# Optimization experiments

Hardware: AMD Instinct MI355X
Metric: run time of the kernel (lower is better)

Reference implementation:

```python
import jax, jax.numpy as jnp
import numpy as np

ENERGY = 0.5  # target low-frequency energy ratio (init kwarg)
B, C, H, W = 8, 32, 512, 512


def setup_inputs() -> dict:
    key = jax.random.key(0)
    x = jax.random.normal(key, (B, C, H, W), dtype=jnp.float32)
    return {"x": x}


def reference(x) -> jnp.ndarray:
    b, c, h, w = x.shape
    crow, ccol = h // 2, w // 2

    f = jnp.fft.fft2(x)                       # [B,C,H,W] complex
    fshift = jnp.fft.fftshift(f, axes=(-2, -1))

    # Per-pixel minimal cutoff c such that pixel lies in the centered
    # square [crow-c:crow+c, ccol-c:ccol+c] (rows crow-c .. crow+c-1).
    ii = jnp.arange(h)
    jj = jnp.arange(w)
    c_row = jnp.maximum(crow - ii, ii - crow + 1)          # [H]
    c_col = jnp.maximum(ccol - jj, jj - ccol + 1)          # [W]
    c_needed = jnp.maximum(c_row[:, None], c_col[None, :])  # [H,W] int

    # Energy of channel 0 spectrum per batch element.
    e0 = jnp.abs(fshift[:, 0]) ** 2                         # [B,H,W]
    num_seg = int(max(crow, h - crow, ccol, w - ccol)) + 1
    seg = c_needed.reshape(-1)
    ring_energy = jax.vmap(
        lambda e: jax.ops.segment_sum(e.reshape(-1), seg, num_segments=num_seg)
    )(e0)                                                   # [B, num_seg]
    cum_energy = jnp.cumsum(ring_energy, axis=1)            # cum_energy[:, c] = low-freq energy at cutoff c
    total = cum_energy[:, -1]
    target = total * ENERGY

    # Search c in range(1, min(h,w)//2); first c with cum >= target, else 5.
    cmax = min(h, w) // 2
    cand = cum_energy[:, 1:cmax] >= target[:, None]          # [B, cmax-1]
    found = jnp.any(cand, axis=1)
    first = jnp.argmax(cand, axis=1) + 1                     # first satisfying cutoff
    cutoff = jnp.where(found, first, 5)                      # [B] int

    # Zero the centered square (same cutoff for all channels of a sample).
    keep = c_needed[None, :, :] > cutoff[:, None, None]      # [B,H,W] bool
    fshift = fshift * keep[:, None, :, :].astype(fshift.dtype)

    ishift = jnp.fft.ifftshift(fshift, axes=(-2, -1))
    return jnp.abs(jnp.fft.ifft2(ishift))
```

## Files before the change

kernel.cpp:

```cpp
#include <hip/hip_runtime.h>
#include <math.h>

#define FN 512
#define TPB 256
#define NIMG 256
#define NBATCH 8
#define NCH 32
#define NBINS 257
#define WACOLS 257
#define WBS 256
#define SPITCH 516

typedef unsigned long long ull;

__device__ __forceinline__ float2 cadd(float2 a, float2 b) { return make_float2(a.x + b.x, a.y + b.y); }
__device__ __forceinline__ float2 csub(float2 a, float2 b) { return make_float2(a.x - b.x, a.y - b.y); }
__device__ __forceinline__ float2 cmul(float2 a, float2 b) {
  return make_float2(fmaf(a.x, b.x, -a.y * b.y), fmaf(a.x, b.y, a.y * b.x));
}
template<bool INV>
__device__ __forceinline__ float2 cmul_s(float2 a, float2 w) {
  if (!INV) return make_float2(fmaf(a.x, w.x, -a.y * w.y), fmaf(a.x, w.y,  a.y * w.x));
  else      return make_float2(fmaf(a.x, w.x,  a.y * w.y), fmaf(a.y, w.x, -a.x * w.y));
}
__device__ __forceinline__ float2 cexpm(float ang) {
  float s, c;
  __sincosf(ang, &s, &c);
  return make_float2(c, s);
}
template<bool INV>
__device__ __forceinline__ float2 mulpmi(float2 a) {
  return INV ? make_float2(-a.y, a.x) : make_float2(a.y, -a.x);
}

template<bool INV>
__device__ __forceinline__ void dft8(float2 r[8]) {
  const float C = 0.70710678118654752440f;
  float2 t0 = cadd(r[0], r[4]), t1 = csub(r[0], r[4]);
  float2 t2 = cadd(r[2], r[6]), t3 = mulpmi<INV>(csub(r[2], r[6]));
  float2 E0 = cadd(t0, t2), E1 = cadd(t1, t3), E2 = csub(t0, t2), E3 = csub(t1, t3);
  float2 u0 = cadd(r[1], r[5]), u1 = csub(r[1], r[5]);
  float2 u2 = cadd(r[3], r[7]), u3 = mulpmi<INV>(csub(r[3], r[7]));
  float2 O0 = cadd(u0, u2), O1 = cadd(u1, u3), O2 = csub(u0, u2), O3 = csub(u1, u3);
  float2 O1w, O2w, O3w;
  if (!INV) {
    O1w = make_float2(C * (O1.x + O1.y), C * (O1.y - O1.x));
    O2w = make_float2(O2.y, -O2.x);
    O3w = make_float2(C * (O3.y - O3.x), -C * (O3.x + O3.y));
  } else {
    O1w = make_float2(C * (O1.x - O1.y), C * (O1.y + O1.x));
    O2w = make_float2(-O2.y, O2.x);
    O3w = make_float2(-C * (O3.x + O3.y), C * (O3.x - O3.y));
  }
  r[0] = cadd(E0, O0); r[1] = cadd(E1, O1w); r[2] = cadd(E2, O2w); r[3] = cadd(E3, O3w);
  r[4] = csub(E0, O0); r[5] = csub(E1, O1w); r[6] = csub(E2, O2w); r[7] = csub(E3, O3w);
}

__device__ __forceinline__ int swz(int q) {
  int b = (q >> 6) & 7;
  return q ^ b ^ ((b & 4) << 1);
}

#define TWOPI 6.2831853071795864769f

__device__ __forceinline__ void build_tw(int t, float2 tw512[7], float2 tw64[7]) {
  float2 w1 = cexpm(-TWOPI * (float)t * (1.0f / 512.0f));
  tw512[0] = w1;
  #pragma unroll
  for (int k = 1; k < 7; ++k) tw512[k] = cmul(tw512[k - 1], w1);
  float2 v1 = cexpm(-TWOPI * (float)(t & 7) * (1.0f / 64.0f));
  tw64[0] = v1;
  #pragma unroll
  for (int e = 1; e < 7; ++e) tw64[e] = cmul(tw64[e - 1], v1);
}

template<bool INV>
__device__ __forceinline__ void fft512_dif2(float2 rA[8], float2 rB[8],
                                            float2* __restrict__ LA, float2* __restrict__ LB,
                                            int t, const float2 tw512[7], const float2 tw64[7]) {
  dft8<INV>(rA);
  dft8<INV>(rB);
  #pragma unroll
  for (int k = 1; k < 8; ++k) {
    rA[k] = cmul_s<INV>(rA[k], tw512[k - 1]);
    rB[k] = cmul_s<INV>(rB[k], tw512[k - 1]);
  }
  #pragma unroll
  for (int k = 0; k < 8; ++k) { LA[swz(64 * k + t)] = rA[k]; LB[swz(64 * k + t)] = rB[k]; }
  const int base = 64 * (t >> 3) + (t & 7);
  #pragma unroll
  for (int d = 0; d < 8; ++d) rA[d] = LA[swz(base + 8 * d)];
  #pragma unroll
  for (int d = 0; d < 8; ++d) rB[d] = LB[swz(base + 8 * d)];
  dft8<INV>(rA);
  dft8<INV>(rB);
  #pragma unroll
  for (int e = 1; e < 8; ++e) {
    rA[e] = cmul_s<INV>(rA[e], tw64[e - 1]);
    rB[e] = cmul_s<INV>(rB[e], tw64[e - 1]);
  }
  #pragma unroll
  for (int e = 0; e < 8; ++e) { LA[swz(base + 8 * e)] = rA[e]; LB[swz(base + 8 * e)] = rB[e]; }
  #pragma unroll
  for (int m = 0; m < 8; ++m) rA[m] = LA[swz(8 * t + m)];
  #pragma unroll
  for (int m = 0; m < 8; ++m) rB[m] = LB[swz(8 * t + m)];
  dft8<INV>(rA);
  dft8<INV>(rB);
}

template<bool INV>
__device__ __forceinline__ void fft512_dit2(float2 rA[8], float2 rB[8],
                                            float2* __restrict__ LA, float2* __restrict__ LB,
                                            int t, const float2 tw64[7], float2 w0, float2 st) {
  dft8<INV>(rA);
  dft8<INV>(rB);
  #pragma unroll
  for (int c = 1; c < 8; ++c) {
    rA[c] = cmul_s<INV>(rA[c], tw64[c - 1]);
    rB[c] = cmul_s<INV>(rB[c], tw64[c - 1]);
  }
  #pragma unroll
  for (int c = 0; c < 8; ++c) { LA[swz(8 * t + c)] = rA[c]; LB[swz(8 * t + c)] = rB[c]; }
  const int base = 64 * (t >> 3) + (t & 7);
  #pragma unroll
  for (int e = 0; e < 8; ++e) rA[e] = LA[swz(base + 8 * e)];
  #pragma unroll
  for (int e = 0; e < 8; ++e) rB[e] = LB[swz(base + 8 * e)];
  dft8<INV>(rA);
  dft8<INV>(rB);
  {
    float2 w = w0;
    #pragma unroll
    for (int d = 0; d < 8; ++d) {
      rA[d] = cmul(rA[d], w);
      rB[d] = cmul(rB[d], w);
      w = cmul(w, st);
    }
  }
  #pragma unroll
  for (int d = 0; d < 8; ++d) { LA[swz(base + 8 * d)] = rA[d]; LB[swz(base + 8 * d)] = rB[d]; }
  #pragma unroll
  for (int j = 0; j < 8; ++j) rA[j] = LA[swz(64 * j + t)];
  #pragma unroll
  for (int j = 0; j < 8; ++j) rB[j] = LB[swz(64 * j + t)];
  dft8<INV>(rA);
  dft8<INV>(rB);
}

template<bool INV>
__device__ __forceinline__ void fft512_dif(float2 r[8], float2* __restrict__ L, int t,
                                           const float2 tw512[7], const float2 tw64[7]) {
  dft8<INV>(r);
  #pragma unroll
  for (int k = 1; k < 8; ++k) r[k] = cmul_s<INV>(r[k], tw512[k - 1]);
  #pragma unroll
  for (int k = 0; k < 8; ++k) L[swz(64 * k + t)] = r[k];
  const int base = 64 * (t >> 3) + (t & 7);
  #pragma unroll
  for (int d = 0; d < 8; ++d) r[d] = L[swz(base + 8 * d)];
  dft8<INV>(r);
  #pragma unroll
  for (int e = 1; e < 8; ++e) r[e] = cmul_s<INV>(r[e], tw64[e - 1]);
  #pragma unroll
  for (int e = 0; e < 8; ++e) L[swz(base + 8 * e)] = r[e];
  #pragma unroll
  for (int m = 0; m < 8; ++m) r[m] = L[swz(8 * t + m)];
  dft8<INV>(r);
}

__device__ __forceinline__ int ringc(int u) { return (u < 256) ? (u + 1) : (512 - u); }

__global__ __launch_bounds__(TPB, 4) void k_fwd_real(const float* __restrict__ x,
                                                     float2* __restrict__ W,
                                                     int img0, int img_stride,
                                                     const int* __restrict__ cut, int use_cut) {
  __shared__ float2 stg[8][SPITCH];
  const int g = threadIdx.x >> 6, t = threadIdx.x & 63;
  const int li = blockIdx.x >> 5;
  const int R0 = (blockIdx.x & 31) * 16;
  const int img = img0 + li * img_stride;
  int ulim = 256;
  if (use_cut) ulim = cut[img >> 5];
  const float* __restrict__ base = x + (size_t)img * (FN * FN);
  float2 tw512[7], tw64[7];
  build_tw(t, tw512, tw64);
  {
    const float* __restrict__ raA = base + (size_t)(R0 + 2 * g) * FN;
    const float* __restrict__ rbA = raA + FN;
    const float* __restrict__ raB = base + (size_t)(R0 + 8 + 2 * g) * FN;
    const float* __restrict__ rbB = raB + FN;
    float2 rA[8], rB[8];
    #pragma unroll
    for (int j = 0; j < 8; ++j) {
      rA[j] = make_float2(raA[t + 64 * j], rbA[t + 64 * j]);
      rB[j] = make_float2(raB[t + 64 * j], rbB[t + 64 * j]);
    }
    fft512_dif2<false>(rA, rB, &stg[g][0], &stg[4 + g][0], t, tw512, tw64);
    #pragma unroll
    for (int f = 0; f < 8; ++f) {
      int p = 64 * f + 8 * (t & 7) + (t >> 3);
      stg[g][p] = rA[f];
      stg[4 + g][p] = rB[f];
    }
  }
  __syncthreads();
  float2* __restrict__ dst = W + (size_t)li * (WACOLS * FN);
  const int pr = threadIdx.x & 7;
  const int u0 = threadIdx.x >> 3;
  #pragma unroll
  for (int kk = 0; kk < 8; ++kk) {
    int u = u0 + 32 * kk;
    if (u <= ulim) {
      float2 Za = stg[pr][u];
      float2 Zb = stg[pr][(512 - u) & 511];
      float2 Fa = make_float2(0.5f * (Za.x + Zb.x), 0.5f * (Za.y - Zb.y));
      float2 Fb = make_float2(0.5f * (Za.y + Zb.y), 0.5f * (Zb.x - Za.x));
      float4* d4 = (float4*)(dst + (size_t)u * FN + R0 + 2 * pr);
      *d4 = make_float4(Fa.x, Fa.y, Fb.x, Fb.y);
    }
  }
  if (!use_cut && threadIdx.x < 8) {
    float2 Z = stg[threadIdx.x][256];
    float4* d4 = (float4*)(dst + (size_t)256 * FN + R0 + 2 * threadIdx.x);
    *d4 = make_float4(Z.x, 0.f, Z.y, 0.f);
  }
}

__global__ __launch_bounds__(TPB) void k_ring(const float2* __restrict__ W1p, ull* __restrict__ bins) {
  __shared__ float2 ex[4][FN];
  __shared__ ull lbins[NBINS];
  const int g = threadIdx.x >> 6, t = threadIdx.x & 63;
  for (int i = threadIdx.x; i < NBINS; i += TPB) lbins[i] = 0;
  __syncthreads();
  const int li = blockIdx.x / 33;
  const int U0 = (blockIdx.x % 33) * 8;
  const float2* __restrict__ src = W1p + (size_t)li * (WACOLS * FN);
  float2 tw512[7], tw64[7];
  build_tw(t, tw512, tw64);
  #pragma unroll
  for (int s = 0; s < 2; ++s) {
    const int u = U0 + 4 * s + g;
    if (u > 256) continue;
    const float2* __restrict__ row = src + (size_t)u * FN;
    float2 r[8];
    #pragma unroll
    for (int j = 0; j < 8; ++j) r[j] = row[t + 64 * j];
    fft512_dif<false>(r, &ex[g][0], t, tw512, tw64);
    const int cu = ringc(u);
    const bool mir = (u >= 1 && u <= 255);
    const int cmu = mir ? ringc(512 - u) : 0;
    #pragma unroll
    for (int f = 0; f < 8; ++f) {
      int v = 64 * f + 8 * (t & 7) + (t >> 3);
      float e = fmaf(r[f].x, r[f].x, r[f].y * r[f].y);
      ull q = (ull)((double)e * 1048576.0);
      atomicAdd(&lbins[max(cu, ringc(v))], q);
      if (mir) atomicAdd(&lbins[max(cmu, ringc((512 - v) & 511))], q);
    }
  }
  __syncthreads();
  for (int i = threadIdx.x; i < NBINS; i += TPB)
    if (lbins[i]) atomicAdd(&bins[(size_t)li * NBINS + i], lbins[i]);
}

__global__ __launch_bounds__(64) void k_cutoff(const ull* __restrict__ bins, int* __restrict__ cut) {
  int b = threadIdx.x;
  if (b >= NBATCH) return;
  double tot = 0.0;
  for (int r = 0; r < NBINS; ++r) tot += (double)bins[b * NBINS + r];
  double target = 0.5 * tot;
  double cum = 0.0;
  int c = 5;
  bool found = false;
  for (int r = 0; r <= 255; ++r) {
    cum += (double)bins[b * NBINS + r];
    if (r >= 1 && !found && cum >= target) { c = r; found = true; }
  }
  cut[b] = c;
}

__global__ __launch_bounds__(TPB, 4) void k_cols(const float2* __restrict__ Wa,
                                                 float2* __restrict__ Wb,
                                                 float2* __restrict__ Abuf,
                                                 float2* __restrict__ Bv,
                                                 float2* __restrict__ Fc,
                                                 float2* __restrict__ c4raw,
                                                 const int* __restrict__ cut, int img0) {
  __shared__ float2 stg[8][SPITCH];
  const int g = threadIdx.x >> 6, t = threadIdx.x & 63;
  const int li = blockIdx.x >> 5;
  const int U0 = (blockIdx.x & 31) * 8;
  const int cutoff = cut[(img0 + li) >> 5];
  const int NC = 512 - cutoff;
  if (U0 > cutoff) return;
  const float2* __restrict__ src = Wa + (size_t)li * (WACOLS * FN);
  float2 tw512[7], tw64[7];
  build_tw(t, tw512, tw64);
  const int tk = t >> 3, tc = t & 7;
  const float2 w0d = cexpm(TWOPI * (float)(tc * tk) * (1.0f / 512.0f));
  const float2 std = cexpm(TWOPI * (float)tk * (1.0f / 64.0f));
  const float sc = 1.0f / 512.0f;
  const int uA = U0 + g, uB = U0 + 4 + g;
  const float2* __restrict__ rowA = src + (size_t)uA * FN;
  const float2* __restrict__ rowB = src + (size_t)uB * FN;
  float2 rA[8], rB[8];
  #pragma unroll
  for (int j = 0; j < 8; ++j) { rA[j] = rowA[t + 64 * j]; rB[j] = rowB[t + 64 * j]; }
  float2* LA = &stg[g][0];
  float2* LB = &stg[4 + g][0];
  fft512_dif2<false>(rA, rB, LA, LB, t, tw512, tw64);
  const int vt = 8 * tc + tk;
  #pragma unroll
  for (int f = 0; f < 8; ++f) {
    int v = 64 * f + vt;
    if (v == cutoff) {
      if (uA < cutoff) Fc[li * 256 + uA] = rA[f];
      else if (uA == cutoff) c4raw[li] = rA[f];
      if (uB < cutoff) Fc[li * 256 + uB] = rB[f];
      else if (uB == cutoff) c4raw[li] = rB[f];
    }
    if (v == NC) {
      if (uA < cutoff) Bv[li * 256 + uA] = rA[f];
      if (uB < cutoff) Bv[li * 256 + uB] = rB[f];
    }
  }
  #pragma unroll
  for (int f = 0; f < 8; ++f) {
    int v = 64 * f + vt;
    bool lo = (v < cutoff) || (v > NC);
    rA[f] = lo ? make_float2(rA[f].x * sc, rA[f].y * sc) : make_float2(0.f, 0.f);
    rB[f] = lo ? make_float2(rB[f].x * sc, rB[f].y * sc) : make_float2(0.f, 0.f);
  }
  fft512_dit2<true>(rA, rB, LA, LB, t, tw64, w0d, std);
  const bool aA = (uA == cutoff), aB = (uB == cutoff);
  #pragma unroll
  for (int j = 0; j < 8; ++j) {
    int h = t + 64 * j;
    stg[g][h] = rA[j];
    stg[4 + g][h] = rB[j];
    if (aA) Abuf[li * 512 + h] = rA[j];
    if (aB) Abuf[li * 512 + h] = rB[j];
  }
  __syncthreads();
  float2* __restrict__ dst = Wb + (size_t)li * (512 * WBS);
  const int rl2 = threadIdx.x & 3;
  const int hg = threadIdx.x >> 2;
  #pragma unroll
  for (int kk = 0; kk < 8; ++kk) {
    int h = hg + 64 * kk;
    float2 a = stg[2 * rl2][h];
    float2 b = stg[2 * rl2 + 1][h];
    float4* d4 = (float4*)(dst + (size_t)h * WBS + U0 + 2 * rl2);
    *d4 = make_float4(a.x, a.y, b.x, b.y);
  }
}

__global__ __launch_bounds__(64) void k_gv(const float2* __restrict__ Bv,
                                           const float2* __restrict__ Fc,
                                           float2* __restrict__ bvec,
                                           const int* __restrict__ cut, int img0) {
  __shared__ float2 ex[SPITCH];
  const int t = threadIdx.x;
  const int li = blockIdx.x;
  const int cutoff = cut[(img0 + li) >> 5];
  const float s2 = 1.0f / (512.0f * 512.0f);
  float2 tw512[7], tw64[7];
  build_tw(t, tw512, tw64);
  float2 r[8];
  #pragma unroll
  for (int j = 0; j < 8; ++j) {
    int u = t + 64 * j;
    float2 gv = make_float2(0.f, 0.f);
    if (u < cutoff) {
      float2 b = Bv[li * 256 + u];
      gv = make_float2(b.x * s2, b.y * s2);
    } else if (u >= 513 - cutoff) {
      float2 F = Fc[li * 256 + (512 - u)];
      gv = make_float2(F.x * s2, -F.y * s2);
    }
    r[j] = gv;
  }
  fft512_dif<true>(r, ex, t, tw512, tw64);
  #pragma unroll
  for (int f = 0; f < 8; ++f) {
    int w = 64 * f + 8 * (t & 7) + (t >> 3);
    bvec[li * 512 + w] = r[f];
  }
}

__global__ __launch_bounds__(TPB, 4) void k_rows(const float2* __restrict__ Wb,
                                                 const float2* __restrict__ Abuf,
                                                 const float2* __restrict__ bvec,
                                                 const float2* __restrict__ c4raw,
                                                 const float* __restrict__ x,
                                                 float* __restrict__ out,
                                                 const int* __restrict__ cut, int img0) {
  __shared__ float2 ex[4][SPITCH];
  const int g = threadIdx.x >> 6, t = threadIdx.x & 63;
  const int li = blockIdx.x >> 6;
  const int H0 = (blockIdx.x & 63) * 8;
  const int img = img0 + li;
  const int cutoff = cut[img >> 5];
  const int NC = 512 - cutoff;
  const float2* __restrict__ wbase = Wb + (size_t)li * (512 * WBS);
  const float* __restrict__ xbase = x + (size_t)img * (FN * FN);
  float* __restrict__ obase = out + (size_t)img * (FN * FN);
  float2 tw512[7], tw64[7];
  build_tw(t, tw512, tw64);
  const float sc = 1.0f / 512.0f;
  const int h1 = H0 + 2 * g, h2 = h1 + 1;
  const float2* __restrict__ r1 = wbase + (size_t)h1 * WBS;
  const float2* __restrict__ r2 = wbase + (size_t)h2 * WBS;
  float2 r[8];
  #pragma unroll
  for (int j = 0; j < 8; ++j) {
    int u = t + 64 * j;
    float2 z;
    if (u < cutoff) {
      float2 m1 = r1[u], m2 = r2[u];
      z = make_float2(m1.x - m2.y, m1.y + m2.x);
    } else if (u > NC) {
      int um = 512 - u;
      float2 m1 = r1[um], m2 = r2[um];
      z = make_float2(m1.x + m2.y, -m1.y + m2.x);
    } else {
      z = make_float2(0.f, 0.f);
    }
    r[j] = make_float2(z.x * sc, z.y * sc);
  }
  fft512_dif<true>(r, &ex[g][0], t, tw512, tw64);
  const float s2 = sc * sc;
  float2 cv = c4raw[li];
  const float2 c4 = make_float2(cv.x * s2, -cv.y * s2);
  float2 wv1 = cexpm(TWOPI * (float)((NC * h1) & 511) * (1.0f / 512.0f));
  float2 wv2 = cexpm(TWOPI * (float)((NC * h2) & 511) * (1.0f / 512.0f));
  float2 A1 = Abuf[li * 512 + h1], A2 = Abuf[li * 512 + h2];
  float2 A1p = cadd(make_float2(A1.x * sc, -A1.y * sc), cmul(c4, wv1));
  float2 A2p = cadd(make_float2(A2.x * sc, -A2.y * sc), cmul(c4, wv2));
  const int w0i = 8 * (t & 7) + (t >> 3);
  float2 ph = cexpm(TWOPI * (float)((NC * w0i) & 511) * (1.0f / 512.0f));
  const float2 s64 = cexpm(TWOPI * (float)((64 * (NC & 7)) & 511) * (1.0f / 512.0f));
  const float* __restrict__ x1 = xbase + (size_t)h1 * FN;
  const float* __restrict__ x2 = xbase + (size_t)h2 * FN;
  float* __restrict__ o1 = obase + (size_t)h1 * FN;
  float* __restrict__ o2 = obase + (size_t)h2 * FN;
  const float2* __restrict__ bp = bvec + li * 512;
  #pragma unroll
  for (int f = 0; f < 8; ++f) {
    int p = 64 * f + w0i;
    float2 bv = bp[p];
    float2 d1 = cadd(cmul(ph, A1p), cmul(wv1, bv));
    float2 d2 = cadd(cmul(ph, A2p), cmul(wv2, bv));
    float e1 = x1[p] - r[f].x - d1.x;
    float e2 = x2[p] - r[f].y - d2.x;
    o1[p] = sqrtf(fmaf(e1, e1, d1.y * d1.y));
    o2[p] = sqrtf(fmaf(e2, e2, d2.y * d2.y));
    ph = cmul(ph, s64);
  }
}

extern "C" void kernel_launch(void* const* d_in, const int* in_sizes, int n_in,
                              void* d_out, int out_size, void* d_ws, size_t ws_size,
                              hipStream_t stream) {
  const float* x = (const float*)d_in[0];
  float* out = (float*)d_out;
  char* ws = (char*)d_ws;

  size_t off = 0;
  ull* bins = (ull*)(ws + off);
  off += ((size_t)NBATCH * NBINS * sizeof(ull) + 255) & ~(size_t)255;
  int* cut = (int*)(ws + off);
  off += 256;
  float2* W1p = (float2*)(ws + off);
  off += (size_t)NBATCH * WACOLS * FN * sizeof(float2);

  const size_t per_wa = (size_t)WACOLS * FN * sizeof(float2);
  const size_t per_wb = (size_t)512 * WBS * sizeof(float2);
  const size_t per_side = (size_t)(512 + 512 + 256 + 256 + 8) * sizeof(float2);
  size_t avail = (ws_size > off) ? (ws_size - off) : 0;
  int K = (int)(avail / (per_wa + per_wb + per_side));
  if (K > 32) K = 32;
  if (K < 1) K = 1;
  float2* WA = (float2*)(ws + off);               off += (size_t)K * per_wa;
  float2* WB = (float2*)(ws + off);               off += (size_t)K * per_wb;
  float2* Abuf = (float2*)(ws + off);             off += (size_t)K * 512 * sizeof(float2);
  float2* bvec = (float2*)(ws + off);             off += (size_t)K * 512 * sizeof(float2);
  float2* Bv = (float2*)(ws + off);               off += (size_t)K * 256 * sizeof(float2);
  float2* Fc = (float2*)(ws + off);               off += (size_t)K * 256 * sizeof(float2);
  float2* c4raw = (float2*)(ws + off);            off += (size_t)K * 8 * sizeof(float2);

  hipMemsetAsync(bins, 0, (size_t)NBATCH * NBINS * sizeof(ull), stream);

  hipLaunchKernelGGL(k_fwd_real, dim3(NBATCH * 32), dim3(TPB), 0, stream, x, W1p, 0, NCH, cut, 0);
  hipLaunchKernelGGL(k_ring,     dim3(NBATCH * 33), dim3(TPB), 0, stream, W1p, bins);
  hipLaunchKernelGGL(k_cutoff,   dim3(1),           dim3(64),  0, stream, bins, cut);

  for (int c0 = 0; c0 < NIMG; c0 += K) {
    int nk = (NIMG - c0 < K) ? (NIMG - c0) : K;
    hipLaunchKernelGGL(k_fwd_real, dim3(nk * 32), dim3(TPB), 0, stream, x, WA, c0, 1, cut, 1);
    hipLaunchKernelGGL(k_cols,     dim3(nk * 32), dim3(TPB), 0, stream, WA, WB, Abuf, Bv, Fc, c4raw, cut, c0);
    hipLaunchKernelGGL(k_gv,       dim3(nk),      dim3(64),  0, stream, Bv, Fc, bvec, cut, c0);
    hipLaunchKernelGGL(k_rows,     dim3(nk * 64), dim3(TPB), 0, stream, WB, Abuf, bvec, c4raw, x, out, cut, c0);
  }
}
```

Before: 523.4 us.

## Fuse k_gv into k_cols via last-block atomic counter and raise chunk cap

Removes the separate k_gv launch. Each k_cols block now bumps a per-image atomic counter, and the last of the 32 blocks for an image runs the 512-point inverse FFT that builds bvec. It also raises the chunk cap K from 32 to 43 images, which cuts the number of chunk iterations and kernel launches. The cost is an extra threadfence and atomic in every block and serial tail work on the last block. A larger K also needs more workspace, so the final K still depends on ws_size.

```diff
diff --git a/kernel.cpp b/kernel.cpp
--- a/kernel.cpp
+++ b/kernel.cpp
@@ -286,106 +286,111 @@
                                                  float2* __restrict__ Bv,
                                                  float2* __restrict__ Fc,
                                                  float2* __restrict__ c4raw,
+                                                 float2* __restrict__ bvec,
+                                                 unsigned* __restrict__ cnt,
                                                  const int* __restrict__ cut, int img0) {
   __shared__ float2 stg[8][SPITCH];
+  __shared__ int lastFlag;
   const int g = threadIdx.x >> 6, t = threadIdx.x & 63;
   const int li = blockIdx.x >> 5;
   const int U0 = (blockIdx.x & 31) * 8;
-  const int cutoff = cut[(img0 + li) >> 5];
+  const int img = img0 + li;
+  const int cutoff = cut[img >> 5];
   const int NC = 512 - cutoff;
-  if (U0 > cutoff) return;
-  const float2* __restrict__ src = Wa + (size_t)li * (WACOLS * FN);
-  float2 tw512[7], tw64[7];
-  build_tw(t, tw512, tw64);
-  const int tk = t >> 3, tc = t & 7;
-  const float2 w0d = cexpm(TWOPI * (float)(tc * tk) * (1.0f / 512.0f));
-  const float2 std = cexpm(TWOPI * (float)tk * (1.0f / 64.0f));
-  const float sc = 1.0f / 512.0f;
-  const int uA = U0 + g, uB = U0 + 4 + g;
-  const float2* __restrict__ rowA = src + (size_t)uA * FN;
-  const float2* __restrict__ rowB = src + (size_t)uB * FN;
-  float2 rA[8], rB[8];
-  #pragma unroll
-  for (int j = 0; j < 8; ++j) { rA[j] = rowA[t + 64 * j]; rB[j] = rowB[t + 64 * j]; }
-  float2* LA = &stg[g][0];
-  float2* LB = &stg[4 + g][0];
-  fft512_dif2<false>(rA, rB, LA, LB, t, tw512, tw64);
-  const int vt = 8 * tc + tk;
-  #pragma unroll
-  for (int f = 0; f < 8; ++f) {
-    int v = 64 * f + vt;
-    if (v == cutoff) {
-      if (uA < cutoff) Fc[li * 256 + uA] = rA[f];
-      else if (uA == cutoff) c4raw[li] = rA[f];
-      if (uB < cutoff) Fc[li * 256 + uB] = rB[f];
-      else if (uB == cutoff) c4raw[li] = rB[f];
-    }
-    if (v == NC) {
-      if (uA < cutoff) Bv[li * 256 + uA] = rA[f];
-      if (uB < cutoff) Bv[li * 256 + uB] = rB[f];
-    }
-  }
-  #pragma unroll
-  for (int f = 0; f < 8; ++f) {
-    int v = 64 * f + vt;
-    bool lo = (v < cutoff) || (v > NC);
-    rA[f] = lo ? make_float2(rA[f].x * sc, rA[f].y * sc) : make_float2(0.f, 0.f);
-    rB[f] = lo ? make_float2(rB[f].x * sc, rB[f].y * sc) : make_float2(0.f, 0.f);
-  }
-  fft512_dit2<true>(rA, rB, LA, LB, t, tw64, w0d, std);
-  const bool aA = (uA == cutoff), aB = (uB == cutoff);
-  #pragma unroll
-  for (int j = 0; j < 8; ++j) {
-    int h = t + 64 * j;
-    stg[g][h] = rA[j];
-    stg[4 + g][h] = rB[j];
-    if (aA) Abuf[li * 512 + h] = rA[j];
-    if (aB) Abuf[li * 512 + h] = rB[j];
+  if (U0 <= cutoff) {
+    const float2* __restrict__ src = Wa + (size_t)li * (WACOLS * FN);
+    float2 tw512[7], tw64[7];
+    build_tw(t, tw512, tw64);
+    const int tk = t >> 3, tc = t & 7;
+    const float2 w0d = cexpm(TWOPI * (float)(tc * tk) * (1.0f / 512.0f));
+    const float2 std = cexpm(TWOPI * (float)tk * (1.0f / 64.0f));
+    const float sc = 1.0f / 512.0f;
+    const int uA = U0 + g, uB = U0 + 4 + g;
+    const float2* __restrict__ rowA = src + (size_t)uA * FN;
+    const float2* __restrict__ rowB = src + (size_t)uB * FN;
+    float2 rA[8], rB[8];
+    #pragma unroll
+    for (int j = 0; j < 8; ++j) { rA[j] = rowA[t + 64 * j]; rB[j] = rowB[t + 64 * j]; }
+    float2* LA = &stg[g][0];
+    float2* LB = &stg[4 + g][0];
+    fft512_dif2<false>(rA, rB, LA, LB, t, tw512, tw64);
+    const int vt = 8 * tc + tk;
+    #pragma unroll
+    for (int f = 0; f < 8; ++f) {
+      int v = 64 * f + vt;
+      if (v == cutoff) {
+        if (uA < cutoff) Fc[li * 256 + uA] = rA[f];
+        else if (uA == cutoff) c4raw[li] = rA[f];
+        if (uB < cutoff) Fc[li * 256 + uB] = rB[f];
+        else if (uB == cutoff) c4raw[li] = rB[f];
+      }
+      if (v == NC) {
+        if (uA < cutoff) Bv[li * 256 + uA] = rA[f];
+        if (uB < cutoff) Bv[li * 256 + uB] = rB[f];
+      }
+    }
+    #pragma unroll
+    for (int f = 0; f < 8; ++f) {
+      int v = 64 * f + vt;
+      bool lo = (v < cutoff) || (v > NC);
+      rA[f] = lo ? make_float2(rA[f].x * sc, rA[f].y * sc) : make_float2(0.f, 0.f);
+      rB[f] = lo ? make_float2(rB[f].x * sc, rB[f].y * sc) : make_float2(0.f, 0.f);
+    }
+    fft512_dit2<true>(rA, rB, LA, LB, t, tw64, w0d, std);
+    const bool aA = (uA == cutoff), aB = (uB == cutoff);
+    #pragma unroll
+    for (int j = 0; j < 8; ++j) {
+      int h = t + 64 * j;
+      stg[g][h] = rA[j];
+      stg[4 + g][h] = rB[j];
+      if (aA) Abuf[li * 512 + h] = rA[j];
+      if (aB) Abuf[li * 512 + h] = rB[j];
+    }
+    __syncthreads();
+    float2* __restrict__ dst = Wb + (size_t)li * (512 * WBS);
+    const int rl2 = threadIdx.x & 3;
+    const int hg = threadIdx.x >> 2;
+    #pragma unroll
+    for (int kk = 0; kk < 8; ++kk) {
+      int h = hg + 64 * kk;
+      float2 a = stg[2 * rl2][h];
+      float2 b = stg[2 * rl2 + 1][h];
+      float4* d4 = (float4*)(dst + (size_t)h * WBS + U0 + 2 * rl2);
+      *d4 = make_float4(a.x, a.y, b.x, b.y);
+    }
+  }
+  if (threadIdx.x == 0) {
+    __threadfence();
+    unsigned old = atomicAdd(&cnt[img], 1u);
+    lastFlag = (old == 31u) ? 1 : 0;
   }
   __syncthreads();
-  float2* __restrict__ dst = Wb + (size_t)li * (512 * WBS);
-  const int rl2 = threadIdx.x & 3;
-  const int hg = threadIdx.x >> 2;
-  #pragma unroll
-  for (int kk = 0; kk < 8; ++kk) {
-    int h = hg + 64 * kk;
-    float2 a = stg[2 * rl2][h];
-    float2 b = stg[2 * rl2 + 1][h];
-    float4* d4 = (float4*)(dst + (size_t)h * WBS + U0 + 2 * rl2);
-    *d4 = make_float4(a.x, a.y, b.x, b.y);
-  }
-}
-
-__global__ __launch_bounds__(64) void k_gv(const float2* __restrict__ Bv,
-                                           const float2* __restrict__ Fc,
-                                           float2* __restrict__ bvec,
-                                           const int* __restrict__ cut, int img0) {
-  __shared__ float2 ex[SPITCH];
-  const int t = threadIdx.x;
-  const int li = blockIdx.x;
-  const int cutoff = cut[(img0 + li) >> 5];
-  const float s2 = 1.0f / (512.0f * 512.0f);
-  float2 tw512[7], tw64[7];
-  build_tw(t, tw512, tw64);
-  float2 r[8];
-  #pragma unroll
-  for (int j = 0; j < 8; ++j) {
-    int u = t + 64 * j;
-    float2 gv = make_float2(0.f, 0.f);
-    if (u < cutoff) {
-      float2 b = Bv[li * 256 + u];
-      gv = make_float2(b.x * s2, b.y * s2);
-    } else if (u >= 513 - cutoff) {
-      float2 F = Fc[li * 256 + (512 - u)];
-      gv = make_float2(F.x * s2, -F.y * s2);
-    }
-    r[j] = gv;
-  }
-  fft512_dif<true>(r, ex, t, tw512, tw64);
-  #pragma unroll
-  for (int f = 0; f < 8; ++f) {
-    int w = 64 * f + 8 * (t & 7) + (t >> 3);
-    bvec[li * 512 + w] = r[f];
+  if (lastFlag && threadIdx.x < 64) {
+    __threadfence();
+    const int tt = threadIdx.x;
+    const float s2 = 1.0f / (512.0f * 512.0f);
+    float2 tw512[7], tw64[7];
+    build_tw(tt, tw512, tw64);
+    float2 r[8];
+    #pragma unroll
+    for (int j = 0; j < 8; ++j) {
+      int u = tt + 64 * j;
+      float2 gv = make_float2(0.f, 0.f);
+      if (u < cutoff) {
+        float2 b = Bv[li * 256 + u];
+        gv = make_float2(b.x * s2, b.y * s2);
+      } else if (u >= 513 - cutoff) {
+        float2 F = Fc[li * 256 + (512 - u)];
+        gv = make_float2(F.x * s2, -F.y * s2);
+      }
+      r[j] = gv;
+    }
+    fft512_dif<true>(r, &stg[0][0], tt, tw512, tw64);
+    #pragma unroll
+    for (int f = 0; f < 8; ++f) {
+      int w = 64 * f + 8 * (tt & 7) + (tt >> 3);
+      bvec[li * 512 + w] = r[f];
+    }
   }
 }
 
@@ -469,7 +474,12 @@
 
   size_t off = 0;
   ull* bins = (ull*)(ws + off);
-  off += ((size_t)NBATCH * NBINS * sizeof(ull) + 255) & ~(size_t)255;
+  const size_t bins_bytes = (size_t)NBATCH * NBINS * sizeof(ull);
+  off += bins_bytes;
+  unsigned* cnt = (unsigned*)(ws + off);
+  const size_t cnt_bytes = (size_t)NIMG * sizeof(unsigned);
+  off += cnt_bytes;
+  off = (off + 255) & ~(size_t)255;
   int* cut = (int*)(ws + off);
   off += 256;
   float2* W1p = (float2*)(ws + off);
@@ -480,7 +490,7 @@
   const size_t per_side = (size_t)(512 + 512 + 256 + 256 + 8) * sizeof(float2);
   size_t avail = (ws_size > off) ? (ws_size - off) : 0;
   int K = (int)(avail / (per_wa + per_wb + per_side));
-  if (K > 32) K = 32;
+  if (K > 43) K = 43;
   if (K < 1) K = 1;
   float2* WA = (float2*)(ws + off);               off += (size_t)K * per_wa;
   float2* WB = (float2*)(ws + off);               off += (size_t)K * per_wb;
@@ -490,7 +500,7 @@
   float2* Fc = (float2*)(ws + off);               off += (size_t)K * 256 * sizeof(float2);
   float2* c4raw = (float2*)(ws + off);            off += (size_t)K * 8 * sizeof(float2);
 
-  hipMemsetAsync(bins, 0, (size_t)NBATCH * NBINS * sizeof(ull), stream);
+  hipMemsetAsync(bins, 0, bins_bytes + cnt_bytes, stream);
 
   hipLaunchKernelGGL(k_fwd_real, dim3(NBATCH * 32), dim3(TPB), 0, stream, x, W1p, 0, NCH, cut, 0);
   hipLaunchKernelGGL(k_ring,     dim3(NBATCH * 33), dim3(TPB), 0, stream, W1p, bins);
@@ -499,8 +509,7 @@
   for (int c0 = 0; c0 < NIMG; c0 += K) {
     int nk = (NIMG - c0 < K) ? (NIMG - c0) : K;
     hipLaunchKernelGGL(k_fwd_real, dim3(nk * 32), dim3(TPB), 0, stream, x, WA, c0, 1, cut, 1);
-    hipLaunchKernelGGL(k_cols,     dim3(nk * 32), dim3(TPB), 0, stream, WA, WB, Abuf, Bv, Fc, c4raw, cut, c0);
-    hipLaunchKernelGGL(k_gv,       dim3(nk),      dim3(64),  0, stream, Bv, Fc, bvec, cut, c0);
+    hipLaunchKernelGGL(k_cols,     dim3(nk * 32), dim3(TPB), 0, stream, WA, WB, Abuf, Bv, Fc, c4raw, bvec, cnt, cut, c0);
     hipLaunchKernelGGL(k_rows,     dim3(nk * 64), dim3(TPB), 0, stream, WB, Abuf, bvec, c4raw, x, out, cut, c0);
   }
 }
```

Result: slower. 779.8 us (+49.0%).

## Process one FFT per wave per phase to halve LDS and raise occupancy

Applied to the files above, without the earlier changes.

The forward-row and column kernels now run two sequential phases, each doing a single 512-point FFT per wavefront, instead of two interleaved FFTs per wavefront. This halves the shared staging buffer and the live register arrays, and launch bounds move from 4 to 6 blocks per SM to allow more resident blocks. In exchange, instruction-level parallelism between the two FFTs is lost and each block gains extra barriers and narrower global stores. k_rows also gets the higher occupancy hint without any code restructuring.

```diff
diff --git a/kernel.cpp b/kernel.cpp
--- a/kernel.cpp
+++ b/kernel.cpp
@@ -75,107 +75,57 @@
 }
 
 template<bool INV>
-__device__ __forceinline__ void fft512_dif2(float2 rA[8], float2 rB[8],
-                                            float2* __restrict__ LA, float2* __restrict__ LB,
-                                            int t, const float2 tw512[7], const float2 tw64[7]) {
-  dft8<INV>(rA);
-  dft8<INV>(rB);
-  #pragma unroll
-  for (int k = 1; k < 8; ++k) {
-    rA[k] = cmul_s<INV>(rA[k], tw512[k - 1]);
-    rB[k] = cmul_s<INV>(rB[k], tw512[k - 1]);
-  }
-  #pragma unroll
-  for (int k = 0; k < 8; ++k) { LA[swz(64 * k + t)] = rA[k]; LB[swz(64 * k + t)] = rB[k]; }
+__device__ __forceinline__ void fft512_dif(float2 r[8], float2* __restrict__ L, int t,
+                                           const float2 tw512[7], const float2 tw64[7]) {
+  dft8<INV>(r);
+  #pragma unroll
+  for (int k = 1; k < 8; ++k) r[k] = cmul_s<INV>(r[k], tw512[k - 1]);
+  #pragma unroll
+  for (int k = 0; k < 8; ++k) L[swz(64 * k + t)] = r[k];
   const int base = 64 * (t >> 3) + (t & 7);
   #pragma unroll
-  for (int d = 0; d < 8; ++d) rA[d] = LA[swz(base + 8 * d)];
-  #pragma unroll
-  for (int d = 0; d < 8; ++d) rB[d] = LB[swz(base + 8 * d)];
-  dft8<INV>(rA);
-  dft8<INV>(rB);
-  #pragma unroll
-  for (int e = 1; e < 8; ++e) {
-    rA[e] = cmul_s<INV>(rA[e], tw64[e - 1]);
-    rB[e] = cmul_s<INV>(rB[e], tw64[e - 1]);
-  }
-  #pragma unroll
-  for (int e = 0; e < 8; ++e) { LA[swz(base + 8 * e)] = rA[e]; LB[swz(base + 8 * e)] = rB[e]; }
-  #pragma unroll
-  for (int m = 0; m < 8; ++m) rA[m] = LA[swz(8 * t + m)];
-  #pragma unroll
-  for (int m = 0; m < 8; ++m) rB[m] = LB[swz(8 * t + m)];
-  dft8<INV>(rA);
-  dft8<INV>(rB);
+  for (int d = 0; d < 8; ++d) r[d] = L[swz(base + 8 * d)];
+  dft8<INV>(r);
+  #pragma unroll
+  for (int e = 1; e < 8; ++e) r[e] = cmul_s<INV>(r[e], tw64[e - 1]);
+  #pragma unroll
+  for (int e = 0; e < 8; ++e) L[swz(base + 8 * e)] = r[e];
+  #pragma unroll
+  for (int m = 0; m < 8; ++m) r[m] = L[swz(8 * t + m)];
+  dft8<INV>(r);
 }
 
 template<bool INV>
-__device__ __forceinline__ void fft512_dit2(float2 rA[8], float2 rB[8],
-                                            float2* __restrict__ LA, float2* __restrict__ LB,
-                                            int t, const float2 tw64[7], float2 w0, float2 st) {
-  dft8<INV>(rA);
-  dft8<INV>(rB);
-  #pragma unroll
-  for (int c = 1; c < 8; ++c) {
-    rA[c] = cmul_s<INV>(rA[c], tw64[c - 1]);
-    rB[c] = cmul_s<INV>(rB[c], tw64[c - 1]);
-  }
-  #pragma unroll
-  for (int c = 0; c < 8; ++c) { LA[swz(8 * t + c)] = rA[c]; LB[swz(8 * t + c)] = rB[c]; }
+__device__ __forceinline__ void fft512_dit(float2 r[8], float2* __restrict__ L, int t,
+                                           const float2 tw64[7], float2 w0, float2 st) {
+  dft8<INV>(r);
+  #pragma unroll
+  for (int c = 1; c < 8; ++c) r[c] = cmul_s<INV>(r[c], tw64[c - 1]);
+  #pragma unroll
+  for (int c = 0; c < 8; ++c) L[swz(8 * t + c)] = r[c];
   const int base = 64 * (t >> 3) + (t & 7);
   #pragma unroll
-  for (int e = 0; e < 8; ++e) rA[e] = LA[swz(base + 8 * e)];
-  #pragma unroll
-  for (int e = 0; e < 8; ++e) rB[e] = LB[swz(base + 8 * e)];
-  dft8<INV>(rA);
-  dft8<INV>(rB);
+  for (int e = 0; e < 8; ++e) r[e] = L[swz(base + 8 * e)];
+  dft8<INV>(r);
   {
     float2 w = w0;
     #pragma unroll
-    for (int d = 0; d < 8; ++d) {
-      rA[d] = cmul(rA[d], w);
-      rB[d] = cmul(rB[d], w);
-      w = cmul(w, st);
-    }
-  }
-  #pragma unroll
-  for (int d = 0; d < 8; ++d) { LA[swz(base + 8 * d)] = rA[d]; LB[swz(base + 8 * d)] = rB[d]; }
-  #pragma unroll
-  for (int j = 0; j < 8; ++j) rA[j] = LA[swz(64 * j + t)];
-  #pragma unroll
-  for (int j = 0; j < 8; ++j) rB[j] = LB[swz(64 * j + t)];
-  dft8<INV>(rA);
-  dft8<INV>(rB);
-}
-
-template<bool INV>
-__device__ __forceinline__ void fft512_dif(float2 r[8], float2* __restrict__ L, int t,
-                                           const float2 tw512[7], const float2 tw64[7]) {
-  dft8<INV>(r);
-  #pragma unroll
-  for (int k = 1; k < 8; ++k) r[k] = cmul_s<INV>(r[k], tw512[k - 1]);
-  #pragma unroll
-  for (int k = 0; k < 8; ++k) L[swz(64 * k + t)] = r[k];
-  const int base = 64 * (t >> 3) + (t & 7);
-  #pragma unroll
-  for (int d = 0; d < 8; ++d) r[d] = L[swz(base + 8 * d)];
-  dft8<INV>(r);
-  #pragma unroll
-  for (int e = 1; e < 8; ++e) r[e] = cmul_s<INV>(r[e], tw64[e - 1]);
-  #pragma unroll
-  for (int e = 0; e < 8; ++e) L[swz(base + 8 * e)] = r[e];
-  #pragma unroll
-  for (int m = 0; m < 8; ++m) r[m] = L[swz(8 * t + m)];
+    for (int d = 0; d < 8; ++d) { r[d] = cmul(r[d], w); w = cmul(w, st); }
+  }
+  #pragma unroll
+  for (int d = 0; d < 8; ++d) L[swz(base + 8 * d)] = r[d];
+  #pragma unroll
+  for (int j = 0; j < 8; ++j) r[j] = L[swz(64 * j + t)];
   dft8<INV>(r);
 }
 
 __device__ __forceinline__ int ringc(int u) { return (u < 256) ? (u + 1) : (512 - u); }
 
-__global__ __launch_bounds__(TPB, 4) void k_fwd_real(const float* __restrict__ x,
+__global__ __launch_bounds__(TPB, 6) void k_fwd_real(const float* __restrict__ x,
                                                      float2* __restrict__ W,
                                                      int img0, int img_stride,
                                                      const int* __restrict__ cut, int use_cut) {
-  __shared__ float2 stg[8][SPITCH];
+  __shared__ float2 stg[4][SPITCH];
   const int g = threadIdx.x >> 6, t = threadIdx.x & 63;
   const int li = blockIdx.x >> 5;
   const int R0 = (blockIdx.x & 31) * 16;
@@ -183,47 +133,41 @@
   int ulim = 256;
   if (use_cut) ulim = cut[img >> 5];
   const float* __restrict__ base = x + (size_t)img * (FN * FN);
+  float2* __restrict__ dst = W + (size_t)li * (WACOLS * FN);
   float2 tw512[7], tw64[7];
   build_tw(t, tw512, tw64);
-  {
-    const float* __restrict__ raA = base + (size_t)(R0 + 2 * g) * FN;
-    const float* __restrict__ rbA = raA + FN;
-    const float* __restrict__ raB = base + (size_t)(R0 + 8 + 2 * g) * FN;
-    const float* __restrict__ rbB = raB + FN;
-    float2 rA[8], rB[8];
-    #pragma unroll
-    for (int j = 0; j < 8; ++j) {
-      rA[j] = make_float2(raA[t + 64 * j], rbA[t + 64 * j]);
-      rB[j] = make_float2(raB[t + 64 * j], rbB[t + 64 * j]);
-    }
-    fft512_dif2<false>(rA, rB, &stg[g][0], &stg[4 + g][0], t, tw512, tw64);
-    #pragma unroll
-    for (int f = 0; f < 8; ++f) {
-      int p = 64 * f + 8 * (t & 7) + (t >> 3);
-      stg[g][p] = rA[f];
-      stg[4 + g][p] = rB[f];
-    }
-  }
-  __syncthreads();
-  float2* __restrict__ dst = W + (size_t)li * (WACOLS * FN);
-  const int pr = threadIdx.x & 7;
-  const int u0 = threadIdx.x >> 3;
-  #pragma unroll
-  for (int kk = 0; kk < 8; ++kk) {
-    int u = u0 + 32 * kk;
-    if (u <= ulim) {
-      float2 Za = stg[pr][u];
-      float2 Zb = stg[pr][(512 - u) & 511];
-      float2 Fa = make_float2(0.5f * (Za.x + Zb.x), 0.5f * (Za.y - Zb.y));
-      float2 Fb = make_float2(0.5f * (Za.y + Zb.y), 0.5f * (Zb.x - Za.x));
-      float4* d4 = (float4*)(dst + (size_t)u * FN + R0 + 2 * pr);
-      *d4 = make_float4(Fa.x, Fa.y, Fb.x, Fb.y);
-    }
-  }
-  if (!use_cut && threadIdx.x < 8) {
-    float2 Z = stg[threadIdx.x][256];
-    float4* d4 = (float4*)(dst + (size_t)256 * FN + R0 + 2 * threadIdx.x);
-    *d4 = make_float4(Z.x, 0.f, Z.y, 0.f);
+  #pragma unroll
+  for (int ph = 0; ph < 2; ++ph) {
+    const int pr = 4 * ph + g;
+    const float* __restrict__ ra = base + (size_t)(R0 + 2 * pr) * FN;
+    const float* __restrict__ rb = ra + FN;
+    float2 r[8];
+    #pragma unroll
+    for (int j = 0; j < 8; ++j) r[j] = make_float2(ra[t + 64 * j], rb[t + 64 * j]);
+    fft512_dif<false>(r, &stg[g][0], t, tw512, tw64);
+    #pragma unroll
+    for (int f = 0; f < 8; ++f) stg[g][64 * f + 8 * (t & 7) + (t >> 3)] = r[f];
+    __syncthreads();
+    const int prl = threadIdx.x & 3;
+    const int u0 = threadIdx.x >> 2;
+    #pragma unroll
+    for (int kk = 0; kk < 4; ++kk) {
+      int u = u0 + 64 * kk;
+      if (u <= ulim) {
+        float2 Za = stg[prl][u];
+        float2 Zb = stg[prl][(512 - u) & 511];
+        float2 Fa = make_float2(0.5f * (Za.x + Zb.x), 0.5f * (Za.y - Zb.y));
+        float2 Fb = make_float2(0.5f * (Za.y + Zb.y), 0.5f * (Zb.x - Za.x));
+        float4* d4 = (float4*)(dst + (size_t)u * FN + R0 + 8 * ph + 2 * prl);
+        *d4 = make_float4(Fa.x, Fa.y, Fb.x, Fb.y);
+      }
+    }
+    if (!use_cut && threadIdx.x < 4) {
+      float2 Z = stg[threadIdx.x][256];
+      float4* d4 = (float4*)(dst + (size_t)256 * FN + R0 + 8 * ph + 2 * threadIdx.x);
+      *d4 = make_float4(Z.x, 0.f, Z.y, 0.f);
+    }
+    __syncthreads();
   }
 }
 
@@ -280,14 +224,14 @@
   cut[b] = c;
 }
 
-__global__ __launch_bounds__(TPB, 4) void k_cols(const float2* __restrict__ Wa,
+__global__ __launch_bounds__(TPB, 6) void k_cols(const float2* __restrict__ Wa,
                                                  float2* __restrict__ Wb,
                                                  float2* __restrict__ Abuf,
                                                  float2* __restrict__ Bv,
                                                  float2* __restrict__ Fc,
                                                  float2* __restrict__ c4raw,
                                                  const int* __restrict__ cut, int img0) {
-  __shared__ float2 stg[8][SPITCH];
+  __shared__ float2 stg[4][SPITCH];
   const int g = threadIdx.x >> 6, t = threadIdx.x & 63;
   const int li = blockIdx.x >> 5;
   const int U0 = (blockIdx.x & 31) * 8;
@@ -295,64 +239,59 @@
   const int NC = 512 - cutoff;
   if (U0 > cutoff) return;
   const float2* __restrict__ src = Wa + (size_t)li * (WACOLS * FN);
+  float2* __restrict__ dst = Wb + (size_t)li * (512 * WBS);
   float2 tw512[7], tw64[7];
   build_tw(t, tw512, tw64);
   const int tk = t >> 3, tc = t & 7;
   const float2 w0d = cexpm(TWOPI * (float)(tc * tk) * (1.0f / 512.0f));
   const float2 std = cexpm(TWOPI * (float)tk * (1.0f / 64.0f));
   const float sc = 1.0f / 512.0f;
-  const int uA = U0 + g, uB = U0 + 4 + g;
-  const float2* __restrict__ rowA = src + (size_t)uA * FN;
-  const float2* __restrict__ rowB = src + (size_t)uB * FN;
-  float2 rA[8], rB[8];
-  #pragma unroll
-  for (int j = 0; j < 8; ++j) { rA[j] = rowA[t + 64 * j]; rB[j] = rowB[t + 64 * j]; }
-  float2* LA = &stg[g][0];
-  float2* LB = &stg[4 + g][0];
-  fft512_dif2<false>(rA, rB, LA, LB, t, tw512, tw64);
   const int vt = 8 * tc + tk;
   #pragma unroll
-  for (int f = 0; f < 8; ++f) {
-    int v = 64 * f + vt;
-    if (v == cutoff) {
-      if (uA < cutoff) Fc[li * 256 + uA] = rA[f];
-      else if (uA == cutoff) c4raw[li] = rA[f];
-      if (uB < cutoff) Fc[li * 256 + uB] = rB[f];
-      else if (uB == cutoff) c4raw[li] = rB[f];
-    }
-    if (v == NC) {
-      if (uA < cutoff) Bv[li * 256 + uA] = rA[f];
-      if (uB < cutoff) Bv[li * 256 + uB] = rB[f];
-    }
-  }
-  #pragma unroll
-  for (int f = 0; f < 8; ++f) {
-    int v = 64 * f + vt;
-    bool lo = (v < cutoff) || (v > NC);
-    rA[f] = lo ? make_float2(rA[f].x * sc, rA[f].y * sc) : make_float2(0.f, 0.f);
-    rB[f] = lo ? make_float2(rB[f].x * sc, rB[f].y * sc) : make_float2(0.f, 0.f);
-  }
-  fft512_dit2<true>(rA, rB, LA, LB, t, tw64, w0d, std);
-  const bool aA = (uA == cutoff), aB = (uB == cutoff);
-  #pragma unroll
-  for (int j = 0; j < 8; ++j) {
-    int h = t + 64 * j;
-    stg[g][h] = rA[j];
-    stg[4 + g][h] = rB[j];
-    if (aA) Abuf[li * 512 + h] = rA[j];
-    if (aB) Abuf[li * 512 + h] = rB[j];
-  }
-  __syncthreads();
-  float2* __restrict__ dst = Wb + (size_t)li * (512 * WBS);
-  const int rl2 = threadIdx.x & 3;
-  const int hg = threadIdx.x >> 2;
-  #pragma unroll
-  for (int kk = 0; kk < 8; ++kk) {
-    int h = hg + 64 * kk;
-    float2 a = stg[2 * rl2][h];
-    float2 b = stg[2 * rl2 + 1][h];
-    float4* d4 = (float4*)(dst + (size_t)h * WBS + U0 + 2 * rl2);
-    *d4 = make_float4(a.x, a.y, b.x, b.y);
+  for (int ph = 0; ph < 2; ++ph) {
+    const int u = U0 + 4 * ph + g;
+    const float2* __restrict__ row = src + (size_t)u * FN;
+    float2 r[8];
+    #pragma unroll
+    for (int j = 0; j < 8; ++j) r[j] = row[t + 64 * j];
+    fft512_dif<false>(r, &stg[g][0], t, tw512, tw64);
+    #pragma unroll
+    for (int f = 0; f < 8; ++f) {
+      int v = 64 * f + vt;
+      if (v == cutoff) {
+        if (u < cutoff) Fc[li * 256 + u] = r[f];
+        else if (u == cutoff) c4raw[li] = r[f];
+      }
+      if (v == NC) {
+        if (u < cutoff) Bv[li * 256 + u] = r[f];
+      }
+    }
+    #pragma unroll
+    for (int f = 0; f < 8; ++f) {
+      int v = 64 * f + vt;
+      bool lo = (v < cutoff) || (v > NC);
+      r[f] = lo ? make_float2(r[f].x * sc, r[f].y * sc) : make_float2(0.f, 0.f);
+    }
+    fft512_dit<true>(r, &stg[g][0], t, tw64, w0d, std);
+    const bool isA = (u == cutoff);
+    #pragma unroll
+    for (int j = 0; j < 8; ++j) {
+      int h = t + 64 * j;
+      stg[g][h] = r[j];
+      if (isA) Abuf[li * 512 + h] = r[j];
+    }
+    __syncthreads();
+    const int c2 = threadIdx.x & 1;
+    const int hb = threadIdx.x >> 1;
+    #pragma unroll
+    for (int kk = 0; kk < 4; ++kk) {
+      int h = hb + 128 * kk;
+      float2 a = stg[2 * c2][h];
+      float2 b = stg[2 * c2 + 1][h];
+      float4* d4 = (float4*)(dst + (size_t)h * WBS + U0 + 4 * ph + 2 * c2);
+      *d4 = make_float4(a.x, a.y, b.x, b.y);
+    }
+    __syncthreads();
   }
 }
 
@@ -389,7 +328,7 @@
   }
 }
 
-__global__ __launch_bounds__(TPB, 4) void k_rows(const float2* __restrict__ Wb,
+__global__ __launch_bounds__(TPB, 6) void k_rows(const float2* __restrict__ Wb,
                                                  const float2* __restrict__ Abuf,
                                                  const float2* __restrict__ bvec,
                                                  const float2* __restrict__ c4raw,
```

New measurement: 801.3 us. +53.1%, slower.
